# Optimization experiments

Measured on AMD Instinct MI355X. Metric: run time of the kernel, lower is better.

The kernel has to match this reference:

```python
import jax, jax.numpy as jnp
import numpy as np

B, N, C, OUT, KD, H, E = 16, 10000, 256, 256, 16, 4, 320000
NIT = 3
DV = OUT // H  # per-head value dim = 64


def setup_inputs() -> dict:
    key = jax.random.key(0)
    ks = jax.random.split(key, 7)
    x = jax.random.normal(ks[0], (B, N, C), dtype=jnp.float32)
    edge_rows = jax.random.randint(ks[1], (E,), 0, N, dtype=jnp.int32)
    edge_cols = jax.random.randint(ks[2], (E,), 0, N, dtype=jnp.int32)
    edge_vals = jax.random.uniform(ks[3], (E,), dtype=jnp.float32)
    s = 1.0 / np.sqrt(C).astype(np.float32)
    # nn.Linear(C, out, bias=False) computes x @ W.T; we store W already transposed as [C, out]
    Wk = jax.random.uniform(ks[4], (C, KD * H), dtype=jnp.float32, minval=-s, maxval=s)
    Wq = jax.random.uniform(ks[5], (C, KD * H), dtype=jnp.float32, minval=-s, maxval=s)
    Wv = jax.random.uniform(ks[6], (C, OUT), dtype=jnp.float32, minval=-s, maxval=s)
    ln_gamma = jnp.ones((DV,), dtype=jnp.float32)
    ln_beta = jnp.zeros((DV,), dtype=jnp.float32)
    return {"x": x, "edge_vals": edge_vals, "Wk": Wk, "Wq": Wq, "Wv": Wv,
            "ln_gamma": ln_gamma, "ln_beta": ln_beta,
            "edge_rows": edge_rows, "edge_cols": edge_cols}


def reference(x, edge_vals, Wk, Wq, Wv, ln_gamma, ln_beta, edge_rows, edge_cols):
    decay = jnp.linspace(0.1, 0.5, H).astype(x.dtype)[None, None, :, None]  # [1,1,H,1]
    k = jax.nn.elu(x @ Wk) + 1.0          # [B, N, H*KD]
    q = jax.nn.elu(x @ Wq) + 1.0          # [B, N, H*KD]
    v = x @ Wv                            # [B, N, OUT]
    k = k.reshape(B, N, H, KD).transpose(1, 0, 2, 3)  # [N, B, H, KD]
    acc = k
    it = k
    for _ in range(1, NIT):
        it = it * decay                                   # per-head decay
        flat = it.reshape(N, B * H * KD)                  # [N, B*H*KD]
        # sparse mm: out[r] += val * flat[c] for each edge (r, c)
        flat = jax.ops.segment_sum(edge_vals[:, None] * flat[edge_cols],
                                   edge_rows, num_segments=N)
        it = flat.reshape(N, B, H, KD)
        acc = acc + it
    k = acc.transpose(1, 0, 2, 3)                         # [B, N, H, KD]
    w = (k * q.reshape(B, N, H, KD)).mean(-1, keepdims=True)  # [B, N, H, 1]
    v = v.reshape(B, N, H, DV) * w
    mu = v.mean(-1, keepdims=True)
    var = jnp.var(v, axis=-1, keepdims=True)  # biased, as torch LayerNorm
    v = (v - mu) * jax.lax.rsqrt(var + 1e-5) * ln_gamma + ln_beta
    # faithful to torch: reshape [B,N,H,DV] row-major into [N,B,OUT], then swap axes
    out = v.reshape(N, B, OUT).swapaxes(0, 1)
    return out
```

## Files before the change

### kernel.cpp

```cpp
#include <hip/hip_runtime.h>

#define Mm 160000
#define Nn 10000

typedef __attribute__((ext_vector_type(8))) short short8;
typedef __attribute__((ext_vector_type(4))) short short4v;
typedef __attribute__((ext_vector_type(4))) float float4v;

__device__ __forceinline__ short f2bf(float f) {
  unsigned u = __builtin_bit_cast(unsigned, f);
  u = (u + 0x7FFFu + ((u >> 16) & 1u)) >> 16;
  return (short)u;
}

__global__ __launch_bounds__(256) void prep_k(const float* __restrict__ Wv,
                                              short* __restrict__ bt) {
  const int n = blockIdx.x, k = threadIdx.x;
  bt[n * 256 + k] = f2bf(Wv[k * 256 + n]);
}

__global__ __launch_bounds__(256) void gemm_ln(const float* __restrict__ x,
                                               const short* __restrict__ bt,
                                               const float* __restrict__ gamma,
                                               const float* __restrict__ beta,
                                               float* __restrict__ out) {
  __shared__ short A[64][72];
  __shared__ short Bt[256][72];
  const int t = threadIdx.x;
  const int m0 = blockIdx.x * 64;
  const int w = t >> 6;
  const int l = t & 63;
  const int c16 = l & 15;
  const int q8 = (l >> 4) * 8;

  float4v acc[4][4];
#pragma unroll
  for (int i = 0; i < 4; ++i)
#pragma unroll
    for (int j = 0; j < 4; ++j) acc[i][j] = (float4v){0.f, 0.f, 0.f, 0.f};

  const int ar = t >> 4, ak = (t & 15) * 4;
  const int bn = t >> 3, bk = (t & 7) * 8;

  for (int k0 = 0; k0 < 256; k0 += 64) {
    __syncthreads();
#pragma unroll
    for (int j = 0; j < 4; ++j) {
      float4 a = *(const float4*)(x + (size_t)(m0 + ar + j * 16) * 256 + k0 + ak);
      short4v s;
      s.x = f2bf(a.x); s.y = f2bf(a.y); s.z = f2bf(a.z); s.w = f2bf(a.w);
      *(short4v*)&A[ar + j * 16][ak] = s;
    }
#pragma unroll
    for (int j = 0; j < 8; ++j) {
      int4 v = *(const int4*)(bt + (size_t)(bn + j * 32) * 256 + k0 + bk);
      *(int4*)&Bt[bn + j * 32][bk] = v;
    }
    __syncthreads();
#pragma unroll
    for (int c = 0; c < 2; ++c) {
      short8 af[4], bf[4];
#pragma unroll
      for (int i = 0; i < 4; ++i)
        af[i] = *(const short8*)&A[i * 16 + c16][c * 32 + q8];
#pragma unroll
      for (int j = 0; j < 4; ++j)
        bf[j] = *(const short8*)&Bt[w * 64 + j * 16 + c16][c * 32 + q8];
#pragma unroll
      for (int i = 0; i < 4; ++i)
#pragma unroll
        for (int j = 0; j < 4; ++j)
          acc[i][j] = __builtin_amdgcn_mfma_f32_16x16x32_bf16(af[i], bf[j],
                                                              acc[i][j], 0, 0, 0);
    }
  }

  float g[4], be[4];
#pragma unroll
  for (int j = 0; j < 4; ++j) {
    g[j] = gamma[j * 16 + c16];
    be[j] = beta[j * 16 + c16];
  }
  const int q4 = (l >> 4) * 4;
#pragma unroll
  for (int i = 0; i < 4; ++i) {
#pragma unroll
    for (int reg = 0; reg < 4; ++reg) {
      float s1 = acc[i][0][reg] + acc[i][1][reg] + acc[i][2][reg] + acc[i][3][reg];
      float s2 = acc[i][0][reg] * acc[i][0][reg] + acc[i][1][reg] * acc[i][1][reg] +
                 acc[i][2][reg] * acc[i][2][reg] + acc[i][3][reg] * acc[i][3][reg];
      s1 += __shfl_xor(s1, 1); s2 += __shfl_xor(s2, 1);
      s1 += __shfl_xor(s1, 2); s2 += __shfl_xor(s2, 2);
      s1 += __shfl_xor(s1, 4); s2 += __shfl_xor(s2, 4);
      s1 += __shfl_xor(s1, 8); s2 += __shfl_xor(s2, 8);
      const float mu = s1 * (1.f / 64.f);
      const float var = s2 * (1.f / 64.f) - mu * mu;
      const float inv = rsqrtf(var + 1e-5f);
      const int m = m0 + i * 16 + q4 + reg;
      const int b = m / Nn;
      const int n = m - b * Nn;
      const size_t obase = (size_t)(n & 15) * 2560000u +
                           (size_t)(b * 625 + (n >> 4)) * 256u + w * 64 + c16;
#pragma unroll
      for (int j = 0; j < 4; ++j)
        out[obase + j * 16] = (acc[i][j][reg] - mu) * inv * g[j] + be[j];
    }
  }
}

extern "C" void kernel_launch(void* const* d_in, const int* in_sizes, int n_in,
                              void* d_out, int out_size, void* d_ws, size_t ws_size,
                              hipStream_t stream) {
  const float* x = (const float*)d_in[0];
  const float* Wv = (const float*)d_in[4];
  const float* gamma = (const float*)d_in[5];
  const float* beta = (const float*)d_in[6];
  float* out = (float*)d_out;
  short* wv_bt = (short*)d_ws;

  prep_k<<<256, 256, 0, stream>>>(Wv, wv_bt);
  gemm_ln<<<Mm / 64, 256, 0, stream>>>(x, wv_bt, gamma, beta, out);
}
```

Measured before the change: 300.9 us.

## Register-prefetch next K tile, load B fragments directly, double-buffer A LDS

```diff
diff --git a/kernel.cpp b/kernel.cpp
--- a/kernel.cpp
+++ b/kernel.cpp
@@ -4,7 +4,6 @@
 #define Nn 10000
 
 typedef __attribute__((ext_vector_type(8))) short short8;
-typedef __attribute__((ext_vector_type(4))) short short4v;
 typedef __attribute__((ext_vector_type(4))) float float4v;
 
 __device__ __forceinline__ short f2bf(float f) {
@@ -13,25 +12,35 @@
   return (short)u;
 }
 
+__device__ __forceinline__ unsigned pack2bf(float a, float b) {
+  unsigned ua = __builtin_bit_cast(unsigned, a);
+  unsigned ub = __builtin_bit_cast(unsigned, b);
+  ua = ua + 0x7FFFu + ((ua >> 16) & 1u);
+  ub = ub + 0x7FFFu + ((ub >> 16) & 1u);
+  return __builtin_amdgcn_perm(ub, ua, 0x07060302);
+}
+
 __global__ __launch_bounds__(256) void prep_k(const float* __restrict__ Wv,
                                               short* __restrict__ bt) {
   const int n = blockIdx.x, k = threadIdx.x;
   bt[n * 256 + k] = f2bf(Wv[k * 256 + n]);
 }
 
-__global__ __launch_bounds__(256) void gemm_ln(const float* __restrict__ x,
-                                               const short* __restrict__ bt,
-                                               const float* __restrict__ gamma,
-                                               const float* __restrict__ beta,
-                                               float* __restrict__ out) {
-  __shared__ short A[64][72];
-  __shared__ short Bt[256][72];
+__global__ __launch_bounds__(256, 3) void gemm_ln(const float* __restrict__ x,
+                                                  const short* __restrict__ bt,
+                                                  const float* __restrict__ gamma,
+                                                  const float* __restrict__ beta,
+                                                  float* __restrict__ out) {
+  __shared__ short A[2][64][72];
   const int t = threadIdx.x;
   const int m0 = blockIdx.x * 64;
-  const int w = t >> 6;
-  const int l = t & 63;
+  const int w = t >> 6, l = t & 63;
   const int c16 = l & 15;
   const int q8 = (l >> 4) * 8;
+  const int ar = t >> 4, ak = (t & 15) * 4;
+
+  const float* xg = x + (size_t)(m0 + ar) * 256 + ak;
+  const short* bg = bt + (size_t)(w * 64 + c16) * 256 + q8;
 
   float4v acc[4][4];
 #pragma unroll
@@ -39,39 +48,56 @@
 #pragma unroll
     for (int j = 0; j < 4; ++j) acc[i][j] = (float4v){0.f, 0.f, 0.f, 0.f};
 
-  const int ar = t >> 4, ak = (t & 15) * 4;
-  const int bn = t >> 3, bk = (t & 7) * 8;
+  float4 a_cur[4], a_nxt[4];
+  short8 b_cur[8], b_nxt[8];
 
-  for (int k0 = 0; k0 < 256; k0 += 64) {
-    __syncthreads();
+#pragma unroll
+  for (int j = 0; j < 4; ++j) a_cur[j] = *(const float4*)(xg + j * 4096);
+#pragma unroll
+  for (int c = 0; c < 2; ++c)
+#pragma unroll
+    for (int j = 0; j < 4; ++j)
+      b_cur[c * 4 + j] = *(const short8*)(bg + j * 4096 + c * 32);
+
+#pragma unroll
+  for (int s = 0; s < 4; ++s) {
+    const int k0 = s * 64;
 #pragma unroll
     for (int j = 0; j < 4; ++j) {
-      float4 a = *(const float4*)(x + (size_t)(m0 + ar + j * 16) * 256 + k0 + ak);
-      short4v s;
-      s.x = f2bf(a.x); s.y = f2bf(a.y); s.z = f2bf(a.z); s.w = f2bf(a.w);
-      *(short4v*)&A[ar + j * 16][ak] = s;
+      uint2 p;
+      p.x = pack2bf(a_cur[j].x, a_cur[j].y);
+      p.y = pack2bf(a_cur[j].z, a_cur[j].w);
+      *(uint2*)&A[s & 1][ar + j * 16][ak] = p;
+    }
+    __syncthreads();
+    if (s < 3) {
+#pragma unroll
+      for (int j = 0; j < 4; ++j)
+        a_nxt[j] = *(const float4*)(xg + (k0 + 64) + j * 4096);
+#pragma unroll
+      for (int c = 0; c < 2; ++c)
+#pragma unroll
+        for (int j = 0; j < 4; ++j)
+          b_nxt[c * 4 + j] = *(const short8*)(bg + (k0 + 64) + j * 4096 + c * 32);
     }
 #pragma unroll
-    for (int j = 0; j < 8; ++j) {
-      int4 v = *(const int4*)(bt + (size_t)(bn + j * 32) * 256 + k0 + bk);
-      *(int4*)&Bt[bn + j * 32][bk] = v;
-    }
-    __syncthreads();
-#pragma unroll
     for (int c = 0; c < 2; ++c) {
-      short8 af[4], bf[4];
+      short8 af[4];
 #pragma unroll
       for (int i = 0; i < 4; ++i)
-        af[i] = *(const short8*)&A[i * 16 + c16][c * 32 + q8];
-#pragma unroll
-      for (int j = 0; j < 4; ++j)
-        bf[j] = *(const short8*)&Bt[w * 64 + j * 16 + c16][c * 32 + q8];
+        af[i] = *(const short8*)&A[s & 1][i * 16 + c16][c * 32 + q8];
 #pragma unroll
       for (int i = 0; i < 4; ++i)
 #pragma unroll
         for (int j = 0; j < 4; ++j)
-          acc[i][j] = __builtin_amdgcn_mfma_f32_16x16x32_bf16(af[i], bf[j],
-                                                              acc[i][j], 0, 0, 0);
+          acc[i][j] = __builtin_amdgcn_mfma_f32_16x16x32_bf16(
+              af[i], b_cur[c * 4 + j], acc[i][j], 0, 0, 0);
+    }
+    if (s < 3) {
+#pragma unroll
+      for (int q = 0; q < 4; ++q) a_cur[q] = a_nxt[q];
+#pragma unroll
+      for (int q = 0; q < 8; ++q) b_cur[q] = b_nxt[q];
     }
   }
 
@@ -103,7 +129,8 @@
                            (size_t)(b * 625 + (n >> 4)) * 256u + w * 64 + c16;
 #pragma unroll
       for (int j = 0; j < 4; ++j)
-        out[obase + j * 16] = (acc[i][j][reg] - mu) * inv * g[j] + be[j];
+        __builtin_nontemporal_store((acc[i][j][reg] - mu) * inv * g[j] + be[j],
+                                    out + obase + j * 16);
     }
   }
 }
```

Result: slower. 322.0 us (+7.0%).
